# Kernel tuning notes

Hardware: AMD Instinct MI355X
Metric: run time of the kernel (lower is better)

Reference implementation:

```python
import jax, jax.numpy as jnp
import numpy as np

LN_EPS = 1e-5
IMPACT_FACTOR = 0.01
IMPACT_DIM = 16


def _layernorm(x, g, b):
    m = x.mean(-1, keepdims=True)
    v = x.var(-1, keepdims=True)
    return (x - m) / jnp.sqrt(v + LN_EPS) * g + b


def setup_inputs() -> dict:
    T, S, H, C, I, B = 50, 100, 256, 100, IMPACT_DIM, 4096
    key = jax.random.key(0)
    ks = jax.random.split(key, 6)
    s0 = jax.random.uniform(ks[0], (B, S), dtype=jnp.float32)
    prices = jax.random.uniform(ks[1], (B, T, S), dtype=jnp.float32)
    # Per-timestep policy params (nn.init.normal_(std=1), biases 0, LayerNorm affine g=1, b=0)
    W1 = jax.random.normal(ks[2], (T, H, S), dtype=jnp.float32)
    W2 = jax.random.normal(ks[3], (T, H, H), dtype=jnp.float32)
    Wo = jax.random.normal(ks[4], (T, C, H), dtype=jnp.float32)
    b1 = jnp.zeros((T, H)); b2 = jnp.zeros((T, H)); bo = jnp.zeros((T, C))
    g1 = jnp.ones((T, H)); be1 = jnp.zeros((T, H))
    g2 = jnp.ones((T, H)); be2 = jnp.zeros((T, H))
    return {"s0": s0, "prices": prices, "W1": W1, "b1": b1, "g1": g1, "be1": be1,
            "W2": W2, "b2": b2, "g2": g2, "be2": be2, "Wo": Wo, "bo": bo}


def reference(s0, prices, W1, b1, g1, be1, W2, b2, g2, be2, Wo, bo):
    B, S = s0.shape
    T = prices.shape[1]
    I = IMPACT_DIM
    # A_mat = impact_factor * eye(S); B_mat, C_mat are zeros (as in the source).
    B_mat = jnp.zeros((S, I), dtype=s0.dtype)
    C_mat = jnp.zeros((I, I), dtype=s0.dtype)
    # xi_t ~ N(0,1) noise drawn each step in the source forward.
    noise = jax.random.normal(jax.random.key(1), (T, B, I), dtype=s0.dtype)

    def policy(p, s):
        w1, bb1, gg1, bbe1, w2, bb2, gg2, bbe2, wo, bbo = p
        x = jax.nn.relu(_layernorm(s @ w1.T + bb1, gg1, bbe1))
        x = jax.nn.relu(_layernorm(x @ w2.T + bb2, gg2, bbe2))
        return x @ wo.T + bbo

    def step(carry, inp):
        s, x, cost = carry
        p_t, params, nz = inp  # p_t: [B,S]
        a = jnp.minimum(policy(params, s), s)
        # P @ (A @ P @ a + B @ x) with A = f*I  ->  p * (f * p * a + x @ B^T)
        impact = p_t * (IMPACT_FACTOR * p_t * a + x @ B_mat.T)
        cost = cost + jnp.sum((p_t + impact) * a, axis=1)
        s = s - a
        x = x @ C_mat.T + nz
        return (s, x, cost), None

    prices_t = jnp.moveaxis(prices, 1, 0)  # [T,B,S]
    params_stack = (W1[:-1], b1[:-1], g1[:-1], be1[:-1],
                    W2[:-1], b2[:-1], g2[:-1], be2[:-1], Wo[:-1], bo[:-1])
    carry0 = (s0, jnp.zeros((B, I), dtype=s0.dtype), jnp.zeros((B,), dtype=s0.dtype))
    (s, x, cost), _ = jax.lax.scan(step, carry0, (prices_t[:-1], params_stack, noise[:-1]))
    # Final step t = T-1: a_t = s_t (liquidate remainder, no policy)
    p_T = prices_t[-1]
    a = s
    impact = p_T * (IMPACT_FACTOR * p_T * a + x @ B_mat.T)
    cost = cost + jnp.sum((p_T + impact) * a, axis=1)
    return cost.mean()
```

## Files before the change

### kernel.cpp

```cpp
#include <hip/hip_runtime.h>
#include <stdint.h>

#define TT 50
#define NSTEP 49
#define NBATCH 4096
#define SS 100
#define HH 256
#define K1 128
#define NO 128
#define MROWS 16
#define NBLK 256
#define NTHR 512

typedef short bf16x8 __attribute__((ext_vector_type(8)));
typedef float f32x4 __attribute__((ext_vector_type(4)));

#define MFMA(a, b, c) __builtin_amdgcn_mfma_f32_16x16x32_bf16((a), (b), (c), 0, 0, 0)

#define G1N (TT * 16 * 4 * 64)
#define G2N (TT * 16 * 8 * 64)
#define G3N (TT * 8 * 8 * 64)

__device__ __forceinline__ void bar_lds() {
  __asm__ volatile("s_waitcnt lgkmcnt(0)\n\ts_barrier" ::: "memory");
}

__device__ __forceinline__ short f2b(float f) {
  union { float f; uint32_t u; } v;
  v.f = f;
  return (short)((v.u + 0x7FFFu + ((v.u >> 16) & 1u)) >> 16);
}

__device__ __forceinline__ bf16x8 cvt8(const float* __restrict__ p) {
  bf16x8 r;
#pragma unroll
  for (int j = 0; j < 8; ++j) r[j] = f2b(p[j]);
  return r;
}

__device__ __forceinline__ bf16x8 ldpad(const float* __restrict__ rowp, int k, int kmax) {
  bf16x8 r;
#pragma unroll
  for (int j = 0; j < 8; ++j) {
    int kk = k + j;
    r[j] = (kk < kmax) ? f2b(rowp[kk]) : (short)0;
  }
  return r;
}

__global__ void zero_out(float* out) {
  if (threadIdx.x == 0 && blockIdx.x == 0) out[0] = 0.f;
}

__global__ void prep(const float* __restrict__ W1, const float* __restrict__ W2,
                     const float* __restrict__ Wo,
                     short* __restrict__ W1g, short* __restrict__ W2g, short* __restrict__ Wog,
                     float* __restrict__ out) {
  const int g = blockIdx.x * blockDim.x + threadIdx.x;
  if (g < G1N) {
    const int t = g >> 12;
    const int rem = g & 4095;
    const int nt = rem >> 8;
    const int ks = (rem >> 6) & 3;
    const int lane = rem & 63;
    const int q = lane >> 4, c16 = lane & 15;
    const int n = nt * 16 + c16;
    const int kb = ks * 32 + q * 8;
    const float* src = W1 + ((size_t)t * HH + n) * SS;
    bf16x8 v;
#pragma unroll
    for (int j = 0; j < 8; ++j) {
      int k = kb + j;
      v[j] = (k < SS) ? f2b(src[k]) : (short)0;
    }
    *(bf16x8*)&W1g[(size_t)g * 8] = v;
  } else if (g < G1N + G2N) {
    const int h = g - G1N;
    const int t = h >> 13;
    const int rem = h & 8191;
    const int nt = rem >> 9;
    const int ks = (rem >> 6) & 7;
    const int lane = rem & 63;
    const int q = lane >> 4, c16 = lane & 15;
    const int n = nt * 16 + c16;
    const int kb = ks * 32 + q * 8;
    const float* src = W2 + ((size_t)t * HH + n) * HH + kb;
    bf16x8 v;
#pragma unroll
    for (int j = 0; j < 8; ++j) v[j] = f2b(src[j]);
    *(bf16x8*)&W2g[(size_t)h * 8] = v;
  } else if (g < G1N + G2N + G3N) {
    const int h = g - G1N - G2N;
    const int t = h >> 12;
    const int rem = h & 4095;
    const int nt = rem >> 9;
    const int ks = (rem >> 6) & 7;
    const int lane = rem & 63;
    const int q = lane >> 4, c16 = lane & 15;
    const int n = nt * 16 + c16;
    const int kb = ks * 32 + q * 8;
    bf16x8 v;
    if (n < SS) {
      const float* src = Wo + ((size_t)t * SS + n) * HH + kb;
#pragma unroll
      for (int j = 0; j < 8; ++j) v[j] = f2b(src[j]);
    } else {
      bf16x8 z = {0, 0, 0, 0, 0, 0, 0, 0};
      v = z;
    }
    *(bf16x8*)&Wog[(size_t)h * 8] = v;
  }
  if (g == 0) out[0] = 0.f;
}

template <int MODE>
__global__ __launch_bounds__(NTHR, 2) void run_kernel(
    const float* __restrict__ s0, const float* __restrict__ prices,
    const float* __restrict__ b1, const float* __restrict__ g1, const float* __restrict__ be1,
    const float* __restrict__ b2, const float* __restrict__ g2, const float* __restrict__ be2,
    const float* __restrict__ bo,
    const float* __restrict__ W1f, const float* __restrict__ W2f, const float* __restrict__ Wof,
    const short* __restrict__ W1g, const short* __restrict__ W2g, const short* __restrict__ Wog,
    float* __restrict__ out) {
  __shared__ short sbuf[MROWS][K1 + 8];
  __shared__ short xb1[MROWS][HH + 8];
  __shared__ short xb2[MROWS][HH + 8];
  __shared__ float lnred[MROWS][17];
  __shared__ float wsum[8];

  const int tid = threadIdx.x;
  const int w = tid >> 6;
  const int lane = tid & 63;
  const int q = lane >> 4;
  const int c16 = lane & 15;
  const int b0 = blockIdx.x * MROWS;

  const int n0 = w * 32 + c16;
  const int n1 = n0 + 16;
  const int col = w * 16 + c16;
  const bool cvalid = col < SS;

  for (int j = tid; j < MROWS * (K1 + 8); j += NTHR) ((short*)sbuf)[j] = 0;
  __syncthreads();

  float s_reg[4];
#pragma unroll
  for (int r = 0; r < 4; ++r) {
    int row = q * 4 + r;
    s_reg[r] = cvalid ? s0[(size_t)(b0 + row) * SS + col] : 0.f;
    if (cvalid) sbuf[row][col] = f2b(s_reg[r]);
  }
  __syncthreads();

  bf16x8 w1f[8];
  auto loadW1 = [&](int t) {
#pragma unroll
    for (int ks = 0; ks < 4; ++ks) {
      if (MODE == 0) {
        w1f[2 * ks + 0] = *(const bf16x8*)&W1g[((((size_t)t * 16 + 2 * w) * 4 + ks) * 64 + lane) * 8];
        w1f[2 * ks + 1] = *(const bf16x8*)&W1g[((((size_t)t * 16 + 2 * w + 1) * 4 + ks) * 64 + lane) * 8];
      } else {
        const int k = ks * 32 + q * 8;
        w1f[2 * ks + 0] = ldpad(W1f + ((size_t)t * HH + n0) * SS, k, SS);
        w1f[2 * ks + 1] = ldpad(W1f + ((size_t)t * HH + n1) * SS, k, SS);
      }
    }
  };
  float pr[4];
  auto loadP = [&](int t) {
#pragma unroll
    for (int r = 0; r < 4; ++r) {
      int row = q * 4 + r;
      pr[r] = cvalid ? prices[((size_t)(b0 + row) * TT + t) * SS + col] : 0.f;
    }
  };

  auto ln_epi = [&](f32x4& a0, f32x4& a1, float bv0, float bv1, float gv0, float gv1,
                    float ev0, float ev1, short (*dst)[HH + 8]) {
    float p1[4], p2[4];
#pragma unroll
    for (int r = 0; r < 4; ++r) {
      float v0 = a0[r] + bv0;
      float v1 = a1[r] + bv1;
      a0[r] = v0;
      a1[r] = v1;
      p1[r] = v0 + v1;
      p2[r] = v0 * v0 + v1 * v1;
    }
#pragma unroll
    for (int m = 1; m <= 8; m <<= 1)
#pragma unroll
      for (int r = 0; r < 4; ++r) {
        p1[r] += __shfl_xor(p1[r], m);
        p2[r] += __shfl_xor(p2[r], m);
      }
    if (c16 == 0) {
#pragma unroll
      for (int r = 0; r < 4; ++r) {
        lnred[q * 4 + r][2 * w] = p1[r];
        lnred[q * 4 + r][2 * w + 1] = p2[r];
      }
    }
    bar_lds();
    float meanv = 0.f, rstdv = 0.f;
    if (lane < 16) {
      float S1 = 0.f, S2 = 0.f;
#pragma unroll
      for (int i = 0; i < 8; ++i) {
        S1 += lnred[lane][2 * i];
        S2 += lnred[lane][2 * i + 1];
      }
      meanv = S1 * (1.f / HH);
      float var = fmaxf(S2 * (1.f / HH) - meanv * meanv, 0.f);
      rstdv = rsqrtf(var + 1e-5f);
    }
#pragma unroll
    for (int r = 0; r < 4; ++r) {
      int row = q * 4 + r;
      float mean = __shfl(meanv, row);
      float rstd = __shfl(rstdv, row);
      float v0 = (a0[r] - mean) * rstd * gv0 + ev0;
      float v1 = (a1[r] - mean) * rstd * gv1 + ev1;
      dst[row][n0] = f2b(fmaxf(v0, 0.f));
      dst[row][n1] = f2b(fmaxf(v1, 0.f));
    }
    bar_lds();
  };

  loadW1(0);
  loadP(0);
  float costreg = 0.f;

  for (int t = 0; t < NSTEP; ++t) {
    const float b1v0 = b1[t * HH + n0], b1v1 = b1[t * HH + n1];
    const float g1v0 = g1[t * HH + n0], g1v1 = g1[t * HH + n1];
    const float e1v0 = be1[t * HH + n0], e1v1 = be1[t * HH + n1];
    const float b2v0 = b2[t * HH + n0], b2v1 = b2[t * HH + n1];
    const float g2v0 = g2[t * HH + n0], g2v1 = g2[t * HH + n1];
    const float e2v0 = be2[t * HH + n0], e2v1 = be2[t * HH + n1];
    const float bov = cvalid ? bo[t * SS + col] : 0.f;

    f32x4 acc0 = (f32x4){0.f, 0.f, 0.f, 0.f};
    f32x4 acc1 = (f32x4){0.f, 0.f, 0.f, 0.f};
#pragma unroll
    for (int ks = 0; ks < 4; ++ks) {
      bf16x8 a = *(const bf16x8*)&sbuf[c16][ks * 32 + q * 8];
      acc0 = MFMA(a, w1f[2 * ks + 0], acc0);
      acc1 = MFMA(a, w1f[2 * ks + 1], acc1);
    }

    bf16x8 w2f[16];
#pragma unroll
    for (int ks = 0; ks < 8; ++ks) {
      if (MODE == 0) {
        w2f[2 * ks + 0] = *(const bf16x8*)&W2g[((((size_t)t * 16 + 2 * w) * 8 + ks) * 64 + lane) * 8];
        w2f[2 * ks + 1] = *(const bf16x8*)&W2g[((((size_t)t * 16 + 2 * w + 1) * 8 + ks) * 64 + lane) * 8];
      } else {
        const int k = ks * 32 + q * 8;
        w2f[2 * ks + 0] = cvt8(W2f + ((size_t)t * HH + n0) * HH + k);
        w2f[2 * ks + 1] = cvt8(W2f + ((size_t)t * HH + n1) * HH + k);
      }
    }

    ln_epi(acc0, acc1, b1v0, b1v1, g1v0, g1v1, e1v0, e1v1, xb1);

    f32x4 acc0b = (f32x4){0.f, 0.f, 0.f, 0.f};
    f32x4 acc1b = (f32x4){0.f, 0.f, 0.f, 0.f};
    acc0 = (f32x4){0.f, 0.f, 0.f, 0.f};
    acc1 = (f32x4){0.f, 0.f, 0.f, 0.f};
#pragma unroll
    for (int ks = 0; ks < 4; ++ks) {
      bf16x8 a = *(const bf16x8*)&xb1[c16][ks * 32 + q * 8];
      acc0 = MFMA(a, w2f[2 * ks + 0], acc0);
      acc1 = MFMA(a, w2f[2 * ks + 1], acc1);
    }
#pragma unroll
    for (int ks = 4; ks < 8; ++ks) {
      bf16x8 a = *(const bf16x8*)&xb1[c16][ks * 32 + q * 8];
      acc0b = MFMA(a, w2f[2 * ks + 0], acc0b);
      acc1b = MFMA(a, w2f[2 * ks + 1], acc1b);
    }
    acc0 = acc0 + acc0b;
    acc1 = acc1 + acc1b;

    bf16x8 wof[8];
#pragma unroll
    for (int ks = 0; ks < 8; ++ks) {
      if (MODE == 0) {
        wof[ks] = *(const bf16x8*)&Wog[((((size_t)t * 8 + w) * 8 + ks) * 64 + lane) * 8];
      } else {
        const int k = ks * 32 + q * 8;
        if (cvalid) {
          wof[ks] = cvt8(Wof + ((size_t)t * SS + col) * HH + k);
        } else {
          bf16x8 z = {0, 0, 0, 0, 0, 0, 0, 0};
          wof[ks] = z;
        }
      }
    }

    ln_epi(acc0, acc1, b2v0, b2v1, g2v0, g2v1, e2v0, e2v1, xb2);

    f32x4 a3 = (f32x4){0.f, 0.f, 0.f, 0.f};
    f32x4 a3b = (f32x4){0.f, 0.f, 0.f, 0.f};
#pragma unroll
    for (int ks = 0; ks < 4; ++ks) {
      bf16x8 a = *(const bf16x8*)&xb2[c16][ks * 32 + q * 8];
      a3 = MFMA(a, wof[ks], a3);
    }
#pragma unroll
    for (int ks = 4; ks < 8; ++ks) {
      bf16x8 a = *(const bf16x8*)&xb2[c16][ks * 32 + q * 8];
      a3b = MFMA(a, wof[ks], a3b);
    }
    a3 = a3 + a3b;

    float pcur[4];
#pragma unroll
    for (int r = 0; r < 4; ++r) pcur[r] = pr[r];
    const int tn = (t + 1 < NSTEP) ? t + 1 : 0;
    loadW1(tn);
    loadP(t + 1);

#pragma unroll
    for (int r = 0; r < 4; ++r) {
      float o = a3[r] + bov;
      float a = fminf(o, s_reg[r]);
      float pa = pcur[r] * a;
      costreg += pa + 0.01f * pa * pa;
      s_reg[r] -= a;
      if (cvalid) sbuf[q * 4 + r][col] = f2b(s_reg[r]);
    }
    bar_lds();
  }

#pragma unroll
  for (int r = 0; r < 4; ++r) {
    float pa = pr[r] * s_reg[r];
    costreg += pa + 0.01f * pa * pa;
  }

#pragma unroll
  for (int m = 1; m < 64; m <<= 1) costreg += __shfl_xor(costreg, m);
  if (lane == 0) wsum[w] = costreg;
  __syncthreads();
  if (tid == 0) {
    float tot = 0.f;
#pragma unroll
    for (int i = 0; i < 8; ++i) tot += wsum[i];
    atomicAdd(out, tot * (1.f / NBATCH));
  }
}

extern "C" void kernel_launch(void* const* d_in, const int* in_sizes, int n_in,
                              void* d_out, int out_size, void* d_ws, size_t ws_size,
                              hipStream_t stream) {
  const float* s0 = (const float*)d_in[0];
  const float* prices = (const float*)d_in[1];
  const float* W1 = (const float*)d_in[2];
  const float* b1 = (const float*)d_in[3];
  const float* g1 = (const float*)d_in[4];
  const float* be1 = (const float*)d_in[5];
  const float* W2 = (const float*)d_in[6];
  const float* b2 = (const float*)d_in[7];
  const float* g2 = (const float*)d_in[8];
  const float* be2 = (const float*)d_in[9];
  const float* Wo = (const float*)d_in[10];
  const float* bo = (const float*)d_in[11];
  float* out = (float*)d_out;

  const size_t need = ((size_t)G1N + G2N + G3N) * 8 * sizeof(short);

  if (ws_size >= need) {
    short* W1g = (short*)d_ws;
    short* W2g = W1g + (size_t)G1N * 8;
    short* Wog = W2g + (size_t)G2N * 8;
    const int ngroups = G1N + G2N + G3N;
    prep<<<dim3((ngroups + 255) / 256), dim3(256), 0, stream>>>(W1, W2, Wo, W1g, W2g, Wog, out);
    run_kernel<0><<<dim3(NBLK), dim3(NTHR), 0, stream>>>(
        s0, prices, b1, g1, be1, b2, g2, be2, bo,
        W1, W2, Wo, W1g, W2g, Wog, out);
  } else {
    zero_out<<<dim3(1), dim3(64), 0, stream>>>(out);
    run_kernel<1><<<dim3(NBLK), dim3(NTHR), 0, stream>>>(
        s0, prices, b1, g1, be1, b2, g2, be2, bo,
        W1, W2, Wo, (const short*)nullptr, (const short*)nullptr, (const short*)nullptr, out);
  }
}
```

Measured before the change: 402.6 us.

## Stage weight conversion through LDS tiles and pin load scheduling in main loop

The prep kernel now uses one workgroup per 16-row weight tile. It loads the tile coalesced into shared memory, then emits the bf16 MFMA fragment layout, so global reads are no longer strided. It also folds b1 into the padded column 100 of W1g, although the main kernel still adds b1 separately and sbuf column 100 is zero, so this has no effect. The main loop gets unroll 1 and sched_barrier pins after the weight prefetch groups, so the compiler keeps the prefetches early and does not sink them toward their use.

```diff
diff --git a/kernel.cpp b/kernel.cpp
--- a/kernel.cpp
+++ b/kernel.cpp
@@ -17,13 +17,17 @@
 
 #define MFMA(a, b, c) __builtin_amdgcn_mfma_f32_16x16x32_bf16((a), (b), (c), 0, 0, 0)
 
-#define G1N (TT * 16 * 4 * 64)
-#define G2N (TT * 16 * 8 * 64)
-#define G3N (TT * 8 * 8 * 64)
+#define W1G_OFF(t, nt, ks) ((((size_t)(t) * 16 + (nt)) * 4 + (ks)) * 512)
+#define W2G_OFF(t, nt, ks) ((((size_t)(t) * 16 + (nt)) * 8 + (ks)) * 512)
+#define WOG_OFF(t, nt, ks) ((((size_t)(t) * 8 + (nt)) * 8 + (ks)) * 512)
+#define N_W1G W1G_OFF(TT, 0, 0)
+#define N_W2G W2G_OFF(TT, 0, 0)
+#define N_WOG WOG_OFF(TT, 0, 0)
 
 __device__ __forceinline__ void bar_lds() {
   __asm__ volatile("s_waitcnt lgkmcnt(0)\n\ts_barrier" ::: "memory");
 }
+__device__ __forceinline__ void pin_loads() { __builtin_amdgcn_sched_barrier(0); }
 
 __device__ __forceinline__ short f2b(float f) {
   union { float f; uint32_t u; } v;
@@ -52,65 +56,68 @@
   if (threadIdx.x == 0 && blockIdx.x == 0) out[0] = 0.f;
 }
 
-__global__ void prep(const float* __restrict__ W1, const float* __restrict__ W2,
-                     const float* __restrict__ Wo,
-                     short* __restrict__ W1g, short* __restrict__ W2g, short* __restrict__ Wog,
-                     float* __restrict__ out) {
-  const int g = blockIdx.x * blockDim.x + threadIdx.x;
-  if (g < G1N) {
-    const int t = g >> 12;
-    const int rem = g & 4095;
-    const int nt = rem >> 8;
-    const int ks = (rem >> 6) & 3;
-    const int lane = rem & 63;
-    const int q = lane >> 4, c16 = lane & 15;
-    const int n = nt * 16 + c16;
-    const int kb = ks * 32 + q * 8;
-    const float* src = W1 + ((size_t)t * HH + n) * SS;
-    bf16x8 v;
-#pragma unroll
-    for (int j = 0; j < 8; ++j) {
-      int k = kb + j;
-      v[j] = (k < SS) ? f2b(src[k]) : (short)0;
-    }
-    *(bf16x8*)&W1g[(size_t)g * 8] = v;
-  } else if (g < G1N + G2N) {
-    const int h = g - G1N;
-    const int t = h >> 13;
-    const int rem = h & 8191;
-    const int nt = rem >> 9;
-    const int ks = (rem >> 6) & 7;
-    const int lane = rem & 63;
-    const int q = lane >> 4, c16 = lane & 15;
-    const int n = nt * 16 + c16;
-    const int kb = ks * 32 + q * 8;
-    const float* src = W2 + ((size_t)t * HH + n) * HH + kb;
-    bf16x8 v;
-#pragma unroll
-    for (int j = 0; j < 8; ++j) v[j] = f2b(src[j]);
-    *(bf16x8*)&W2g[(size_t)h * 8] = v;
-  } else if (g < G1N + G2N + G3N) {
-    const int h = g - G1N - G2N;
-    const int t = h >> 12;
-    const int rem = h & 4095;
-    const int nt = rem >> 9;
-    const int ks = (rem >> 6) & 7;
-    const int lane = rem & 63;
-    const int q = lane >> 4, c16 = lane & 15;
-    const int n = nt * 16 + c16;
-    const int kb = ks * 32 + q * 8;
-    bf16x8 v;
-    if (n < SS) {
-      const float* src = Wo + ((size_t)t * SS + n) * HH + kb;
-#pragma unroll
-      for (int j = 0; j < 8; ++j) v[j] = f2b(src[j]);
-    } else {
-      bf16x8 z = {0, 0, 0, 0, 0, 0, 0, 0};
-      v = z;
-    }
-    *(bf16x8*)&Wog[(size_t)h * 8] = v;
-  }
-  if (g == 0) out[0] = 0.f;
+__global__ __launch_bounds__(256) void prep(
+    const float* __restrict__ W1, const float* __restrict__ b1,
+    const float* __restrict__ W2, const float* __restrict__ Wo,
+    short* __restrict__ W1g, short* __restrict__ W2g, short* __restrict__ Wog,
+    float* __restrict__ out) {
+  __shared__ float tile[16 * 264];
+  const int tid = threadIdx.x;
+  const int wg = blockIdx.x;
+  if (wg == 0 && tid == 0) out[0] = 0.f;
+  if (wg < 800) {
+    const int t = wg >> 4, nt = wg & 15;
+    const float* src = W1 + ((size_t)t * HH + nt * 16) * SS;
+    const float* bsrc = b1 + t * HH + nt * 16;
+    for (int i = tid; i < 16 * K1; i += 256) {
+      int m = i >> 7, k = i & 127;
+      float v = (k < SS) ? src[m * SS + k] : (k == SS ? bsrc[m] : 0.f);
+      tile[m * 264 + k] = v;
+    }
+    __syncthreads();
+    {
+      int ks = tid >> 6, lane = tid & 63;
+      int qq = lane >> 4, cc = lane & 15;
+      bf16x8 v;
+#pragma unroll
+      for (int j = 0; j < 8; ++j) v[j] = f2b(tile[cc * 264 + ks * 32 + qq * 8 + j]);
+      *(bf16x8*)&W1g[W1G_OFF(t, nt, ks) + lane * 8] = v;
+    }
+  } else if (wg < 1600) {
+    const int h = wg - 800;
+    const int t = h >> 4, nt = h & 15;
+    const float* src = W2 + ((size_t)t * HH + nt * 16) * HH;
+    for (int i = tid; i < 16 * HH; i += 256) {
+      int m = i >> 8, k = i & 255;
+      tile[m * 264 + k] = src[m * HH + k];
+    }
+    __syncthreads();
+    for (int gi = tid; gi < 512; gi += 256) {
+      int ks = gi >> 6, lane = gi & 63;
+      int qq = lane >> 4, cc = lane & 15;
+      bf16x8 v;
+#pragma unroll
+      for (int j = 0; j < 8; ++j) v[j] = f2b(tile[cc * 264 + ks * 32 + qq * 8 + j]);
+      *(bf16x8*)&W2g[W2G_OFF(t, nt, ks) + lane * 8] = v;
+    }
+  } else {
+    const int h = wg - 1600;
+    const int t = h >> 3, nt = h & 7;
+    for (int i = tid; i < 16 * HH; i += 256) {
+      int m = i >> 8, k = i & 255;
+      int n = nt * 16 + m;
+      tile[m * 264 + k] = (n < SS) ? Wo[((size_t)t * SS + n) * HH + k] : 0.f;
+    }
+    __syncthreads();
+    for (int gi = tid; gi < 512; gi += 256) {
+      int ks = gi >> 6, lane = gi & 63;
+      int qq = lane >> 4, cc = lane & 15;
+      bf16x8 v;
+#pragma unroll
+      for (int j = 0; j < 8; ++j) v[j] = f2b(tile[cc * 264 + ks * 32 + qq * 8 + j]);
+      *(bf16x8*)&Wog[WOG_OFF(t, nt, ks) + lane * 8] = v;
+    }
+  }
 }
 
 template <int MODE>
@@ -157,8 +164,8 @@
 #pragma unroll
     for (int ks = 0; ks < 4; ++ks) {
       if (MODE == 0) {
-        w1f[2 * ks + 0] = *(const bf16x8*)&W1g[((((size_t)t * 16 + 2 * w) * 4 + ks) * 64 + lane) * 8];
-        w1f[2 * ks + 1] = *(const bf16x8*)&W1g[((((size_t)t * 16 + 2 * w + 1) * 4 + ks) * 64 + lane) * 8];
+        w1f[2 * ks + 0] = *(const bf16x8*)&W1g[W1G_OFF(t, 2 * w, ks) + lane * 8];
+        w1f[2 * ks + 1] = *(const bf16x8*)&W1g[W1G_OFF(t, 2 * w + 1, ks) + lane * 8];
       } else {
         const int k = ks * 32 + q * 8;
         w1f[2 * ks + 0] = ldpad(W1f + ((size_t)t * HH + n0) * SS, k, SS);
@@ -231,6 +238,7 @@
   loadP(0);
   float costreg = 0.f;
 
+#pragma unroll 1
   for (int t = 0; t < NSTEP; ++t) {
     const float b1v0 = b1[t * HH + n0], b1v1 = b1[t * HH + n1];
     const float g1v0 = g1[t * HH + n0], g1v1 = g1[t * HH + n1];
@@ -253,14 +261,15 @@
 #pragma unroll
     for (int ks = 0; ks < 8; ++ks) {
       if (MODE == 0) {
-        w2f[2 * ks + 0] = *(const bf16x8*)&W2g[((((size_t)t * 16 + 2 * w) * 8 + ks) * 64 + lane) * 8];
-        w2f[2 * ks + 1] = *(const bf16x8*)&W2g[((((size_t)t * 16 + 2 * w + 1) * 8 + ks) * 64 + lane) * 8];
+        w2f[2 * ks + 0] = *(const bf16x8*)&W2g[W2G_OFF(t, 2 * w, ks) + lane * 8];
+        w2f[2 * ks + 1] = *(const bf16x8*)&W2g[W2G_OFF(t, 2 * w + 1, ks) + lane * 8];
       } else {
         const int k = ks * 32 + q * 8;
         w2f[2 * ks + 0] = cvt8(W2f + ((size_t)t * HH + n0) * HH + k);
         w2f[2 * ks + 1] = cvt8(W2f + ((size_t)t * HH + n1) * HH + k);
       }
     }
+    pin_loads();
 
     ln_epi(acc0, acc1, b1v0, b1v1, g1v0, g1v1, e1v0, e1v1, xb1);
 
@@ -287,7 +296,7 @@
 #pragma unroll
     for (int ks = 0; ks < 8; ++ks) {
       if (MODE == 0) {
-        wof[ks] = *(const bf16x8*)&Wog[((((size_t)t * 8 + w) * 8 + ks) * 64 + lane) * 8];
+        wof[ks] = *(const bf16x8*)&Wog[WOG_OFF(t, w, ks) + lane * 8];
       } else {
         const int k = ks * 32 + q * 8;
         if (cvalid) {
@@ -298,6 +307,7 @@
         }
       }
     }
+    pin_loads();
 
     ln_epi(acc0, acc1, b2v0, b2v1, g2v0, g2v1, e2v0, e2v1, xb2);
 
@@ -321,6 +331,7 @@
     const int tn = (t + 1 < NSTEP) ? t + 1 : 0;
     loadW1(tn);
     loadP(t + 1);
+    pin_loads();
 
 #pragma unroll
     for (int r = 0; r < 4; ++r) {
@@ -369,14 +380,13 @@
   const float* bo = (const float*)d_in[11];
   float* out = (float*)d_out;
 
-  const size_t need = ((size_t)G1N + G2N + G3N) * 8 * sizeof(short);
+  const size_t need = (N_W1G + N_W2G + N_WOG) * sizeof(short);
 
   if (ws_size >= need) {
     short* W1g = (short*)d_ws;
-    short* W2g = W1g + (size_t)G1N * 8;
-    short* Wog = W2g + (size_t)G2N * 8;
-    const int ngroups = G1N + G2N + G3N;
-    prep<<<dim3((ngroups + 255) / 256), dim3(256), 0, stream>>>(W1, W2, Wo, W1g, W2g, Wog, out);
+    short* W2g = W1g + N_W1G;
+    short* Wog = W2g + N_W2G;
+    prep<<<dim3(2000), dim3(256), 0, stream>>>(W1, b1, W2, Wo, W1g, W2g, Wog, out);
     run_kernel<0><<<dim3(NBLK), dim3(NTHR), 0, stream>>>(
         s0, prices, b1, g1, be1, b2, g2, be2, bo,
         W1, W2, Wo, W1g, W2g, Wog, out);
```

New measurement: 403.9 us. Within noise of the previous version (+0.3%).
